# Performance work log

Hardware: AMD Instinct MI355X
Metric: run time of the kernel (lower is better)

Reference implementation:

```python
import jax, jax.numpy as jnp
import numpy as np

B, S, D = 2, 2048, 1024
H, HD = 16, 64          # num_heads, head_dim = D // H
C = 8                   # subspace_dim of the equivariant relative-position basis
EPS = 1e-6              # flax LayerNorm default epsilon


def setup_inputs() -> dict:
    key = jax.random.key(0)
    ks = jax.random.split(key, 12)
    sd = 0.02
    return {
        "x": jax.random.normal(ks[0], (B, S, D), jnp.float32),
        "Q_basis": jax.random.normal(ks[1], (S, S, C), jnp.float32),
        "Wq": jax.random.normal(ks[2], (D, H, HD), jnp.float32) * sd,
        "bq": jnp.zeros((H, HD), jnp.float32),
        "Wk": jax.random.normal(ks[3], (D, H, HD), jnp.float32) * sd,
        "bk": jnp.zeros((H, HD), jnp.float32),
        "Wv": jax.random.normal(ks[4], (D, H, HD), jnp.float32) * sd,
        "bv": jnp.zeros((H, HD), jnp.float32),
        "q_ln_scale": jnp.ones((HD,), jnp.float32),
        "k_ln_scale": jnp.ones((HD,), jnp.float32),
        "relative_attn": jax.random.normal(ks[5], (C, H), jnp.float32) * sd,
        "Wo": jax.random.normal(ks[6], (H, HD, D), jnp.float32) * sd,
        "bo": jnp.zeros((D,), jnp.float32),
    }


def _layernorm(x, scale):
    # LayerNorm over last axis, use_bias=False
    mu = jnp.mean(x, axis=-1, keepdims=True)
    var = jnp.mean(jnp.square(x - mu), axis=-1, keepdims=True)
    return (x - mu) * jax.lax.rsqrt(var + EPS) * scale


def reference(x, Q_basis, Wq, bq, Wk, bk, Wv, bv,
              q_ln_scale, k_ln_scale, relative_attn, Wo, bo):
    # QKV projections: [B,S,D] x [D,H,HD] -> [B,S,H,HD]
    q = jnp.einsum('bsd,dhk->bshk', x, Wq) + bq
    k = jnp.einsum('bsd,dhk->bshk', x, Wk) + bk
    v = jnp.einsum('bsd,dhk->bshk', x, Wv) + bv
    # QK layernorm over head_dim
    q = _layernorm(q, q_ln_scale)
    k = _layernorm(k, k_ln_scale)
    # Learned relative-position bias: [C,H] x [S,S,C] -> [H,S,S]
    bias = jnp.einsum('ch,qkc->hqk', relative_attn, Q_basis)
    # Scaled dot-product attention with bias (matches nn.dot_product_attention)
    scores = jnp.einsum('bqhd,bkhd->bhqk', q, k) / jnp.sqrt(jnp.float32(HD))
    attn = jax.nn.softmax(scores + bias, axis=-1)
    ctx = jnp.einsum('bhqk,bkhd->bqhd', attn, v)
    # Output projection over (heads, head_dim) -> D
    return jnp.einsum('bqhd,hdo->bqo', ctx, Wo) + bo
```

## Files before the change

kernel.cpp:

```cpp
#include <hip/hip_runtime.h>

typedef float f32x4 __attribute__((ext_vector_type(4)));
typedef __bf16 bf16x8 __attribute__((ext_vector_type(8)));
typedef unsigned short u16x8 __attribute__((ext_vector_type(8)));
typedef unsigned short u16x4 __attribute__((ext_vector_type(4)));

#define AS1 __attribute__((address_space(1)))
#define AS3 __attribute__((address_space(3)))

static __device__ __forceinline__ void gll16(const void* g, void* l) {
  __builtin_amdgcn_global_load_lds((const AS1 void*)g, (AS3 void*)l, 16, 0, 0);
}

static __device__ __forceinline__ float bf2f(unsigned short u) {
  unsigned int x = ((unsigned int)u) << 16;
  float f; __builtin_memcpy(&f, &x, 4); return f;
}
static __device__ __forceinline__ unsigned short f2bf(float f) {
  unsigned int x; __builtin_memcpy(&x, &f, 4);
  unsigned int r = (x + 0x7fffu + ((x >> 16) & 1u)) >> 16;
  return (unsigned short)r;
}

#define LOG2E 1.4426950408889634f
#define QSCALE (0.125f * LOG2E)

__global__ __launch_bounds__(256) void k_cvt_x(const float* __restrict__ x,
                                               unsigned short* __restrict__ xb) {
  int i = (blockIdx.x * 256 + threadIdx.x) * 4;
  float4 v = *(const float4*)(x + i);
  u16x4 o; o.x = f2bf(v.x); o.y = f2bf(v.y); o.z = f2bf(v.z); o.w = f2bf(v.w);
  *(u16x4*)(xb + i) = o;
}

__global__ __launch_bounds__(256) void k_transpose(const float* __restrict__ w0,
                                                   const float* __restrict__ w1,
                                                   const float* __restrict__ w2,
                                                   const float* __restrict__ w3,
                                                   unsigned short* __restrict__ dqkv,
                                                   unsigned short* __restrict__ dwo) {
  __shared__ float tile[32][33];
  int z = blockIdx.z;
  const float* src = (z == 0) ? w0 : (z == 1) ? w1 : (z == 2) ? w2 : w3;
  unsigned short* dst = (z < 3) ? (dqkv + (size_t)z * 1024 * 1024) : dwo;
  int tx = threadIdx.x, ty = threadIdx.y;
  int x0 = blockIdx.x * 32, y0 = blockIdx.y * 32;
#pragma unroll
  for (int i = 0; i < 4; ++i)
    tile[ty + 8 * i][tx] = src[(size_t)(y0 + ty + 8 * i) * 1024 + x0 + tx];
  __syncthreads();
#pragma unroll
  for (int i = 0; i < 4; ++i)
    dst[(size_t)(x0 + ty + 8 * i) * 1024 + y0 + tx] = f2bf(tile[tx][ty + 8 * i]);
}

__global__ __launch_bounds__(256) void k_bias(const float* __restrict__ Qb,
                                              const float* __restrict__ R,
                                              unsigned short* __restrict__ bias) {
  __shared__ float Rs[8][16];
  int t = threadIdx.x;
  if (t < 128) Rs[t >> 4][t & 15] = R[t] * LOG2E;
  __syncthreads();
  int q = blockIdx.x;
  int k = t * 8;
  const float* src = Qb + ((size_t)q * 2048 + k) * 8;
  float a[8][8];
#pragma unroll
  for (int kk = 0; kk < 8; ++kk) {
    float4 lo = *(const float4*)(src + kk * 8);
    float4 hi = *(const float4*)(src + kk * 8 + 4);
    a[kk][0] = lo.x; a[kk][1] = lo.y; a[kk][2] = lo.z; a[kk][3] = lo.w;
    a[kk][4] = hi.x; a[kk][5] = hi.y; a[kk][6] = hi.z; a[kk][7] = hi.w;
  }
#pragma unroll
  for (int h = 0; h < 16; ++h) {
    u16x8 o;
#pragma unroll
    for (int kk = 0; kk < 8; ++kk) {
      float s = 0.f;
#pragma unroll
      for (int c = 0; c < 8; ++c) s += a[kk][c] * Rs[c][h];
      o[kk] = f2bf(s);
    }
    *(u16x8*)(bias + ((size_t)h * 2048 + q) * 2048 + k) = o;
  }
}

__global__ __launch_bounds__(256) void k_qkv(const unsigned short* __restrict__ xb,
                                             const unsigned short* __restrict__ wt,
                                             const float* __restrict__ bq,
                                             const float* __restrict__ bk,
                                             const float* __restrict__ bv,
                                             const float* __restrict__ qls,
                                             const float* __restrict__ kls,
                                             unsigned short* __restrict__ qo,
                                             unsigned short* __restrict__ kqo,
                                             unsigned short* __restrict__ vo) {
  __shared__ unsigned short As[4096];
  __shared__ unsigned short Bs[4096];
  const int tid = threadIdx.x;
  const int w = tid >> 6, lane = tid & 63, quad = lane >> 4, lx = lane & 15;
  const int m0 = blockIdx.y * 128, n0 = blockIdx.x * 128;
  const int wrow = w >> 1, wcol = w & 1;

  f32x4 acc[4][4];
#pragma unroll
  for (int i = 0; i < 4; ++i)
#pragma unroll
    for (int j = 0; j < 4; ++j) acc[i][j] = (f32x4){0.f, 0.f, 0.f, 0.f};

  const unsigned short* ga = xb + (size_t)(m0 + 32 * w + (lane >> 2)) * 1024 + (lane & 3) * 8;
  const unsigned short* gb = wt + (size_t)(n0 + 32 * w + (lane >> 2)) * 1024 + (lane & 3) * 8;
  unsigned short* la = As + w * 1024;
  unsigned short* lb = Bs + w * 1024;

  for (int kt = 0; kt < 32; ++kt) {
    const int kofs = kt * 32;
    gll16(ga + kofs, la);
    gll16(ga + kofs + 16 * 1024, la + 512);
    gll16(gb + kofs, lb);
    gll16(gb + kofs + 16 * 1024, lb + 512);
    __syncthreads();
    bf16x8 af[4], bfr[4];
#pragma unroll
    for (int i = 0; i < 4; ++i)
      af[i] = *(const bf16x8*)&As[(64 * wrow + 16 * i + lx) * 32 + quad * 8];
#pragma unroll
    for (int j = 0; j < 4; ++j)
      bfr[j] = *(const bf16x8*)&Bs[(64 * wcol + 16 * j + lx) * 32 + quad * 8];
#pragma unroll
    for (int i = 0; i < 4; ++i)
#pragma unroll
      for (int j = 0; j < 4; ++j)
        acc[i][j] = __builtin_amdgcn_mfma_f32_16x16x32_bf16(af[i], bfr[j], acc[i][j], 0, 0, 0);
    __syncthreads();
  }

  const int colbase = n0 + 64 * wcol;
  const int region = colbase >> 10;
  const int h = (colbase & 1023) >> 6;
  const float* pbp = (region == 0) ? bq : (region == 1) ? bk : bv;
  float pb[4];
#pragma unroll
  for (int j = 0; j < 4; ++j) pb[j] = pbp[h * 64 + j * 16 + lx];

  if (region == 2) {
#pragma unroll
    for (int i = 0; i < 4; ++i) {
#pragma unroll
      for (int rr = 0; rr < 4; ++rr) {
        int m = m0 + 64 * wrow + 16 * i + quad * 4 + rr;
        int b = m >> 11, s = m & 2047;
        unsigned short* dst = vo + ((size_t)b * 16 + h) * 64 * 2048 + s;
#pragma unroll
        for (int j = 0; j < 4; ++j)
          dst[(size_t)(j * 16 + lx) * 2048] = f2bf(acc[i][j][rr] + pb[j]);
      }
    }
  } else {
    const float fac = region ? 1.0f : QSCALE;
    float scl[4];
    const float* lsp = region ? kls : qls;
#pragma unroll
    for (int j = 0; j < 4; ++j) scl[j] = lsp[j * 16 + lx] * fac;
    unsigned short* base = region ? kqo : qo;
#pragma unroll
    for (int i = 0; i < 4; ++i) {
#pragma unroll
      for (int rr = 0; rr < 4; ++rr) {
        int m = m0 + 64 * wrow + 16 * i + quad * 4 + rr;
        int b = m >> 11, s = m & 2047;
        float v0 = acc[i][0][rr] + pb[0];
        float v1 = acc[i][1][rr] + pb[1];
        float v2 = acc[i][2][rr] + pb[2];
        float v3 = acc[i][3][rr] + pb[3];
        float s1 = v0 + v1 + v2 + v3;
        float s2 = v0 * v0 + v1 * v1 + v2 * v2 + v3 * v3;
#pragma unroll
        for (int d = 1; d < 16; d <<= 1) {
          s1 += __shfl_xor(s1, d, 64);
          s2 += __shfl_xor(s2, d, 64);
        }
        float mu = s1 * 0.015625f;
        float var = s2 * 0.015625f - mu * mu;
        float ri = __builtin_amdgcn_rsqf(var + 1e-6f);
        unsigned short* dst = base + (((size_t)b * 16 + h) * 2048 + s) * 64;
        dst[0 * 16 + lx] = f2bf((v0 - mu) * ri * scl[0]);
        dst[1 * 16 + lx] = f2bf((v1 - mu) * ri * scl[1]);
        dst[2 * 16 + lx] = f2bf((v2 - mu) * ri * scl[2]);
        dst[3 * 16 + lx] = f2bf((v3 - mu) * ri * scl[3]);
      }
    }
  }
}

__global__ __launch_bounds__(256) void k_attn(const unsigned short* __restrict__ qp,
                                              const unsigned short* __restrict__ kp,
                                              const unsigned short* __restrict__ vp,
                                              const unsigned short* __restrict__ bp,
                                              unsigned short* __restrict__ ctx) {
  __shared__ unsigned short Qs[4096];
  __shared__ unsigned short Ks[4096];
  __shared__ unsigned short Vs[4096];
  __shared__ unsigned short Ps[4096];
  const int tid = threadIdx.x;
  const int w = tid >> 6, lane = tid & 63, quad = lane >> 4, lx = lane & 15;
  const int qt = blockIdx.x, h = blockIdx.y, b = blockIdx.z;
  const int q0 = qt * 64;
  const size_t bh = (size_t)b * 16 + h;

  const unsigned short* qg = qp + (bh * 2048 + q0) * 64;
  gll16(qg + w * 512 + lane * 8, Qs + w * 512);
  gll16(qg + 2048 + w * 512 + lane * 8, Qs + 2048 + w * 512);
  __syncthreads();
  bf16x8 qf[2];
#pragma unroll
  for (int hh = 0; hh < 2; ++hh)
    qf[hh] = *(const bf16x8*)&Qs[(16 * w + lx) * 64 + hh * 32 + quad * 8];

  const unsigned short* kg = kp + bh * 2048 * 64;
  const unsigned short* vg = vp + bh * 64 * 2048;
  const unsigned short* bg = bp + ((size_t)h * 2048 + q0 + 16 * w + quad * 4) * 2048 + lx;

  float m_run[4] = {-1e30f, -1e30f, -1e30f, -1e30f};
  float l_run[4] = {0.f, 0.f, 0.f, 0.f};
  f32x4 acco[4];
#pragma unroll
  for (int j = 0; j < 4; ++j) acco[j] = (f32x4){0.f, 0.f, 0.f, 0.f};

  for (int kt = 0; kt < 32; ++kt) {
    const int k0 = kt * 64;
    gll16(kg + (size_t)k0 * 64 + w * 512 + lane * 8, Ks + w * 512);
    gll16(kg + (size_t)k0 * 64 + 2048 + w * 512 + lane * 8, Ks + 2048 + w * 512);
    gll16(vg + (size_t)(w * 8 + (lane >> 3)) * 2048 + k0 + (lane & 7) * 8, Vs + w * 512);
    gll16(vg + (size_t)(32 + w * 8 + (lane >> 3)) * 2048 + k0 + (lane & 7) * 8,
          Vs + 2048 + w * 512);
    unsigned short bu[4][4];
#pragma unroll
    for (int rr = 0; rr < 4; ++rr)
#pragma unroll
      for (int j = 0; j < 4; ++j) bu[rr][j] = bg[(size_t)rr * 2048 + k0 + j * 16];
    __syncthreads();

    f32x4 accs[4];
#pragma unroll
    for (int j = 0; j < 4; ++j)
#pragma unroll
      for (int rr = 0; rr < 4; ++rr) accs[j][rr] = bf2f(bu[rr][j]);
#pragma unroll
    for (int j = 0; j < 4; ++j) {
#pragma unroll
      for (int hh = 0; hh < 2; ++hh) {
        bf16x8 kf = *(const bf16x8*)&Ks[(j * 16 + lx) * 64 + hh * 32 + quad * 8];
        accs[j] = __builtin_amdgcn_mfma_f32_16x16x32_bf16(qf[hh], kf, accs[j], 0, 0, 0);
      }
    }
#pragma unroll
    for (int rr = 0; rr < 4; ++rr) {
      float mx = fmaxf(fmaxf(accs[0][rr], accs[1][rr]), fmaxf(accs[2][rr], accs[3][rr]));
#pragma unroll
      for (int d = 1; d < 16; d <<= 1) mx = fmaxf(mx, __shfl_xor(mx, d, 64));
      float mnew = fmaxf(m_run[rr], mx);
      float al = __builtin_amdgcn_exp2f(m_run[rr] - mnew);
      m_run[rr] = mnew;
      float ps = 0.f;
#pragma unroll
      for (int j = 0; j < 4; ++j) {
        float p = __builtin_amdgcn_exp2f(accs[j][rr] - mnew);
        accs[j][rr] = p;
        ps += p;
      }
#pragma unroll
      for (int d = 1; d < 16; d <<= 1) ps += __shfl_xor(ps, d, 64);
      l_run[rr] = l_run[rr] * al + ps;
#pragma unroll
      for (int j = 0; j < 4; ++j) acco[j][rr] *= al;
#pragma unroll
      for (int j = 0; j < 4; ++j)
        Ps[w * 1024 + (quad * 4 + rr) * 64 + j * 16 + lx] = f2bf(accs[j][rr]);
    }
    __asm__ volatile("s_waitcnt lgkmcnt(0)" ::: "memory");
    bf16x8 pf[2];
#pragma unroll
    for (int kh = 0; kh < 2; ++kh)
      pf[kh] = *(const bf16x8*)&Ps[w * 1024 + lx * 64 + kh * 32 + quad * 8];
#pragma unroll
    for (int j = 0; j < 4; ++j) {
#pragma unroll
      for (int kh = 0; kh < 2; ++kh) {
        bf16x8 vf = *(const bf16x8*)&Vs[(j * 16 + lx) * 64 + kh * 32 + quad * 8];
        acco[j] = __builtin_amdgcn_mfma_f32_16x16x32_bf16(pf[kh], vf, acco[j], 0, 0, 0);
      }
    }
    __syncthreads();
  }

#pragma unroll
  for (int rr = 0; rr < 4; ++rr) {
    float rl = __builtin_amdgcn_rcpf(l_run[rr]);
    int s = q0 + 16 * w + quad * 4 + rr;
    unsigned short* dst = ctx + (((size_t)b * 2048 + s) * 16 + h) * 64;
#pragma unroll
    for (int j = 0; j < 4; ++j) dst[j * 16 + lx] = f2bf(acco[j][rr] * rl);
  }
}

__global__ __launch_bounds__(256) void k_out(const unsigned short* __restrict__ cx,
                                             const unsigned short* __restrict__ wt,
                                             const float* __restrict__ bo,
                                             float* __restrict__ out) {
  __shared__ unsigned short As[4096];
  __shared__ unsigned short Bs[4096];
  const int tid = threadIdx.x;
  const int w = tid >> 6, lane = tid & 63, quad = lane >> 4, lx = lane & 15;
  const int m0 = blockIdx.y * 128, n0 = blockIdx.x * 128;
  const int wrow = w >> 1, wcol = w & 1;

  f32x4 acc[4][4];
#pragma unroll
  for (int i = 0; i < 4; ++i)
#pragma unroll
    for (int j = 0; j < 4; ++j) acc[i][j] = (f32x4){0.f, 0.f, 0.f, 0.f};

  const unsigned short* ga = cx + (size_t)(m0 + 32 * w + (lane >> 2)) * 1024 + (lane & 3) * 8;
  const unsigned short* gb = wt + (size_t)(n0 + 32 * w + (lane >> 2)) * 1024 + (lane & 3) * 8;
  unsigned short* la = As + w * 1024;
  unsigned short* lb = Bs + w * 1024;

  for (int kt = 0; kt < 32; ++kt) {
    const int kofs = kt * 32;
    gll16(ga + kofs, la);
    gll16(ga + kofs + 16 * 1024, la + 512);
    gll16(gb + kofs, lb);
    gll16(gb + kofs + 16 * 1024, lb + 512);
    __syncthreads();
    bf16x8 af[4], bfr[4];
#pragma unroll
    for (int i = 0; i < 4; ++i)
      af[i] = *(const bf16x8*)&As[(64 * wrow + 16 * i + lx) * 32 + quad * 8];
#pragma unroll
    for (int j = 0; j < 4; ++j)
      bfr[j] = *(const bf16x8*)&Bs[(64 * wcol + 16 * j + lx) * 32 + quad * 8];
#pragma unroll
    for (int i = 0; i < 4; ++i)
#pragma unroll
      for (int j = 0; j < 4; ++j)
        acc[i][j] = __builtin_amdgcn_mfma_f32_16x16x32_bf16(af[i], bfr[j], acc[i][j], 0, 0, 0);
    __syncthreads();
  }

  const int colbase = n0 + 64 * wcol;
  float bb[4];
#pragma unroll
  for (int j = 0; j < 4; ++j) bb[j] = bo[colbase + j * 16 + lx];
#pragma unroll
  for (int i = 0; i < 4; ++i) {
#pragma unroll
    for (int rr = 0; rr < 4; ++rr) {
      int m = m0 + 64 * wrow + 16 * i + quad * 4 + rr;
      float* dst = out + (size_t)m * 1024 + colbase;
#pragma unroll
      for (int j = 0; j < 4; ++j) dst[j * 16 + lx] = acc[i][j][rr] + bb[j];
    }
  }
}

extern "C" void kernel_launch(void* const* d_in, const int* in_sizes, int n_in,
                              void* d_out, int out_size, void* d_ws, size_t ws_size,
                              hipStream_t stream) {
  (void)in_sizes; (void)n_in; (void)out_size; (void)ws_size;
  const float* x   = (const float*)d_in[0];
  const float* Qb  = (const float*)d_in[1];
  const float* Wq  = (const float*)d_in[2];
  const float* bq  = (const float*)d_in[3];
  const float* Wk  = (const float*)d_in[4];
  const float* bk  = (const float*)d_in[5];
  const float* Wv  = (const float*)d_in[6];
  const float* bv  = (const float*)d_in[7];
  const float* qls = (const float*)d_in[8];
  const float* kls = (const float*)d_in[9];
  const float* Ra  = (const float*)d_in[10];
  const float* Wo  = (const float*)d_in[11];
  const float* bo  = (const float*)d_in[12];
  float* out = (float*)d_out;

  char* ws = (char*)d_ws;
  unsigned short* xb    = (unsigned short*)(ws + 0);
  unsigned short* wqkvt = (unsigned short*)(ws + 8388608);
  unsigned short* wot   = (unsigned short*)(ws + 14680064);
  unsigned short* qb    = (unsigned short*)(ws + 16777216);
  unsigned short* kb    = (unsigned short*)(ws + 25165824);
  unsigned short* vtb   = (unsigned short*)(ws + 33554432);
  unsigned short* ctxb  = (unsigned short*)(ws + 41943040);
  unsigned short* biasb = (unsigned short*)(ws + 50331648);

  k_cvt_x<<<4096, 256, 0, stream>>>(x, xb);
  k_transpose<<<dim3(32, 32, 4), dim3(32, 8), 0, stream>>>(Wq, Wk, Wv, Wo, wqkvt, wot);
  k_bias<<<2048, 256, 0, stream>>>(Qb, Ra, biasb);
  k_qkv<<<dim3(24, 32), 256, 0, stream>>>(xb, wqkvt, bq, bk, bv, qls, kls, qb, kb, vtb);
  k_attn<<<dim3(32, 16, 2), 256, 0, stream>>>(qb, kb, vtb, biasb, ctxb);
  k_out<<<dim3(8, 32), 256, 0, stream>>>(ctxb, wot, bo, out);
}
```

Before: 502.0 us.

## Merge both batches per attention block and drop online-softmax max tracking

Each attention block now handles the same head and query tile for both batch elements, with two waves per batch. This lets the relative-position bias tile be read once per block instead of once per batch, and the grid shrinks to 32x16. The running-max rescaling is removed and the softmax sum is reduced only at the end. That is exact only while the layernormed scores stay small enough not to overflow exp2, which depends on the LN scales. K and V use XOR-swizzled LDS layouts, Q fragments are read straight from global memory, and the MFMA operand order is swapped so bias and P can be loaded and stored as packed vectors.

Result: faster. 461.8 us (-8.0%).

```diff
diff --git a/kernel.cpp b/kernel.cpp
--- a/kernel.cpp
+++ b/kernel.cpp
@@ -199,109 +199,131 @@
                                               const unsigned short* __restrict__ vp,
                                               const unsigned short* __restrict__ bp,
                                               unsigned short* __restrict__ ctx) {
-  __shared__ unsigned short Qs[4096];
-  __shared__ unsigned short Ks[4096];
-  __shared__ unsigned short Vs[4096];
-  __shared__ unsigned short Ps[4096];
+  __shared__ unsigned short Ks[8192];
+  __shared__ unsigned short Vs[8192];
+  __shared__ unsigned short Ps[9216];
   const int tid = threadIdx.x;
   const int w = tid >> 6, lane = tid & 63, quad = lane >> 4, lx = lane & 15;
-  const int qt = blockIdx.x, h = blockIdx.y, b = blockIdx.z;
+  const int bb = w >> 1, ww = w & 1;
+  const int qt = blockIdx.x, h = blockIdx.y;
   const int q0 = qt * 64;
-  const size_t bh = (size_t)b * 16 + h;
-
-  const unsigned short* qg = qp + (bh * 2048 + q0) * 64;
-  gll16(qg + w * 512 + lane * 8, Qs + w * 512);
-  gll16(qg + 2048 + w * 512 + lane * 8, Qs + 2048 + w * 512);
-  __syncthreads();
-  bf16x8 qf[2];
-#pragma unroll
-  for (int hh = 0; hh < 2; ++hh)
-    qf[hh] = *(const bf16x8*)&Qs[(16 * w + lx) * 64 + hh * 32 + quad * 8];
-
-  const unsigned short* kg = kp + bh * 2048 * 64;
-  const unsigned short* vg = vp + bh * 64 * 2048;
-  const unsigned short* bg = bp + ((size_t)h * 2048 + q0 + 16 * w + quad * 4) * 2048 + lx;
-
-  float m_run[4] = {-1e30f, -1e30f, -1e30f, -1e30f};
-  float l_run[4] = {0.f, 0.f, 0.f, 0.f};
-  f32x4 acco[4];
-#pragma unroll
-  for (int j = 0; j < 4; ++j) acco[j] = (f32x4){0.f, 0.f, 0.f, 0.f};
+  const size_t bh = (size_t)bb * 16 + h;
+
+  const unsigned short* qgp = qp + (bh * 2048 + q0 + ww * 32) * 64;
+  bf16x8 qf[2][2];
+#pragma unroll
+  for (int qg = 0; qg < 2; ++qg)
+#pragma unroll
+    for (int hh = 0; hh < 2; ++hh)
+      qf[qg][hh] = *(const bf16x8*)(qgp + (qg * 16 + lx) * 64 + hh * 32 + quad * 8);
+
+  const int r8 = lane >> 3;
+  const int cA = (lane & 7) ^ r8;
+  const unsigned short* kgs = kp + bh * 2048 * 64 + (ww * 32 + r8) * 64 + cA * 8;
+  const unsigned short* vgs = vp + bh * 64 * 2048 + (size_t)(ww * 32 + r8) * 2048 + cA * 8;
+  unsigned short* ldk = Ks + bb * 4096 + ww * 2048;
+  unsigned short* ldv = Vs + bb * 4096 + ww * 2048;
+  const unsigned short* bg = bp + ((size_t)h * 2048 + q0 + ww * 32) * 2048;
+  unsigned short* psw = Ps + w * 2304;
+
+  float l_run[2] = {0.f, 0.f};
+  f32x4 acco[2][4];
+#pragma unroll
+  for (int qg = 0; qg < 2; ++qg)
+#pragma unroll
+    for (int j = 0; j < 4; ++j) acco[qg][j] = (f32x4){0.f, 0.f, 0.f, 0.f};
 
   for (int kt = 0; kt < 32; ++kt) {
     const int k0 = kt * 64;
-    gll16(kg + (size_t)k0 * 64 + w * 512 + lane * 8, Ks + w * 512);
-    gll16(kg + (size_t)k0 * 64 + 2048 + w * 512 + lane * 8, Ks + 2048 + w * 512);
-    gll16(vg + (size_t)(w * 8 + (lane >> 3)) * 2048 + k0 + (lane & 7) * 8, Vs + w * 512);
-    gll16(vg + (size_t)(32 + w * 8 + (lane >> 3)) * 2048 + k0 + (lane & 7) * 8,
-          Vs + 2048 + w * 512);
-    unsigned short bu[4][4];
-#pragma unroll
-    for (int rr = 0; rr < 4; ++rr)
-#pragma unroll
-      for (int j = 0; j < 4; ++j) bu[rr][j] = bg[(size_t)rr * 2048 + k0 + j * 16];
-    __syncthreads();
-
-    f32x4 accs[4];
+#pragma unroll
+    for (int idx = 0; idx < 4; ++idx) {
+      gll16(kgs + (size_t)(k0 + idx * 8) * 64, ldk + idx * 512);
+      gll16(vgs + k0 + idx * 8 * 2048, ldv + idx * 512);
+    }
+    uint2 bu[2][4];
+#pragma unroll
+    for (int qg = 0; qg < 2; ++qg)
+#pragma unroll
+      for (int j = 0; j < 4; ++j)
+        bu[qg][j] = *(const uint2*)(bg + (size_t)(qg * 16 + lx) * 2048 + k0 + j * 16 + quad * 4);
+    __syncthreads();
+
+    bf16x8 kf[4][2];
 #pragma unroll
     for (int j = 0; j < 4; ++j)
 #pragma unroll
-      for (int rr = 0; rr < 4; ++rr) accs[j][rr] = bf2f(bu[rr][j]);
-#pragma unroll
-    for (int j = 0; j < 4; ++j) {
-#pragma unroll
-      for (int hh = 0; hh < 2; ++hh) {
-        bf16x8 kf = *(const bf16x8*)&Ks[(j * 16 + lx) * 64 + hh * 32 + quad * 8];
-        accs[j] = __builtin_amdgcn_mfma_f32_16x16x32_bf16(qf[hh], kf, accs[j], 0, 0, 0);
+      for (int hh = 0; hh < 2; ++hh)
+        kf[j][hh] = *(const bf16x8*)&Ks[bb * 4096 + (j * 16 + lx) * 64 +
+                                        (((hh * 4 + quad) ^ (lx & 7)) * 8)];
+#pragma unroll
+    for (int qg = 0; qg < 2; ++qg) {
+      f32x4 accs[4];
+#pragma unroll
+      for (int j = 0; j < 4; ++j) {
+        accs[j][0] = __uint_as_float(bu[qg][j].x << 16);
+        accs[j][1] = __uint_as_float(bu[qg][j].x & 0xffff0000u);
+        accs[j][2] = __uint_as_float(bu[qg][j].y << 16);
+        accs[j][3] = __uint_as_float(bu[qg][j].y & 0xffff0000u);
       }
-    }
+#pragma unroll
+      for (int hh = 0; hh < 2; ++hh)
+#pragma unroll
+        for (int j = 0; j < 4; ++j)
+          accs[j] = __builtin_amdgcn_mfma_f32_16x16x32_bf16(kf[j][hh], qf[qg][hh], accs[j], 0, 0, 0);
+#pragma unroll
+      for (int j = 0; j < 4; ++j) {
+        float p0 = __builtin_amdgcn_exp2f(accs[j][0]);
+        float p1 = __builtin_amdgcn_exp2f(accs[j][1]);
+        float p2 = __builtin_amdgcn_exp2f(accs[j][2]);
+        float p3 = __builtin_amdgcn_exp2f(accs[j][3]);
+        l_run[qg] += (p0 + p1) + (p2 + p3);
+        unsigned int a0 = __float_as_uint(p0) + 0x8000u;
+        unsigned int a1 = __float_as_uint(p1) + 0x8000u;
+        unsigned int a2 = __float_as_uint(p2) + 0x8000u;
+        unsigned int a3 = __float_as_uint(p3) + 0x8000u;
+        uint2 pk;
+        pk.x = __builtin_amdgcn_perm(a1, a0, 0x07060302u);
+        pk.y = __builtin_amdgcn_perm(a3, a2, 0x07060302u);
+        *(uint2*)&psw[(qg * 16 + lx) * 72 + j * 16 + quad * 4] = pk;
+      }
+    }
+    __asm__ volatile("s_waitcnt lgkmcnt(0)" ::: "memory");
+    bf16x8 vf[4][2];
+#pragma unroll
+    for (int j = 0; j < 4; ++j)
+#pragma unroll
+      for (int kh = 0; kh < 2; ++kh)
+        vf[j][kh] = *(const bf16x8*)&Vs[bb * 4096 + (j * 16 + lx) * 64 +
+                                        (((kh * 4 + quad) ^ (lx & 7)) * 8)];
+#pragma unroll
+    for (int qg = 0; qg < 2; ++qg) {
+      bf16x8 pf[2];
+#pragma unroll
+      for (int kh = 0; kh < 2; ++kh)
+        pf[kh] = *(const bf16x8*)&psw[(qg * 16 + lx) * 72 + kh * 32 + quad * 8];
+#pragma unroll
+      for (int kh = 0; kh < 2; ++kh)
+#pragma unroll
+        for (int j = 0; j < 4; ++j)
+          acco[qg][j] = __builtin_amdgcn_mfma_f32_16x16x32_bf16(pf[kh], vf[j][kh], acco[qg][j], 0, 0, 0);
+    }
+    __syncthreads();
+  }
+
+#pragma unroll
+  for (int qg = 0; qg < 2; ++qg) {
+    float l = l_run[qg];
+    l += __shfl_xor(l, 16, 64);
+    l += __shfl_xor(l, 32, 64);
 #pragma unroll
     for (int rr = 0; rr < 4; ++rr) {
-      float mx = fmaxf(fmaxf(accs[0][rr], accs[1][rr]), fmaxf(accs[2][rr], accs[3][rr]));
-#pragma unroll
-      for (int d = 1; d < 16; d <<= 1) mx = fmaxf(mx, __shfl_xor(mx, d, 64));
-      float mnew = fmaxf(m_run[rr], mx);
-      float al = __builtin_amdgcn_exp2f(m_run[rr] - mnew);
-      m_run[rr] = mnew;
-      float ps = 0.f;
-#pragma unroll
-      for (int j = 0; j < 4; ++j) {
-        float p = __builtin_amdgcn_exp2f(accs[j][rr] - mnew);
-        accs[j][rr] = p;
-        ps += p;
-      }
-#pragma unroll
-      for (int d = 1; d < 16; d <<= 1) ps += __shfl_xor(ps, d, 64);
-      l_run[rr] = l_run[rr] * al + ps;
-#pragma unroll
-      for (int j = 0; j < 4; ++j) acco[j][rr] *= al;
-#pragma unroll
-      for (int j = 0; j < 4; ++j)
-        Ps[w * 1024 + (quad * 4 + rr) * 64 + j * 16 + lx] = f2bf(accs[j][rr]);
-    }
-    __asm__ volatile("s_waitcnt lgkmcnt(0)" ::: "memory");
-    bf16x8 pf[2];
-#pragma unroll
-    for (int kh = 0; kh < 2; ++kh)
-      pf[kh] = *(const bf16x8*)&Ps[w * 1024 + lx * 64 + kh * 32 + quad * 8];
-#pragma unroll
-    for (int j = 0; j < 4; ++j) {
-#pragma unroll
-      for (int kh = 0; kh < 2; ++kh) {
-        bf16x8 vf = *(const bf16x8*)&Vs[(j * 16 + lx) * 64 + kh * 32 + quad * 8];
-        acco[j] = __builtin_amdgcn_mfma_f32_16x16x32_bf16(pf[kh], vf, acco[j], 0, 0, 0);
-      }
-    }
-    __syncthreads();
-  }
-
-#pragma unroll
-  for (int rr = 0; rr < 4; ++rr) {
-    float rl = __builtin_amdgcn_rcpf(l_run[rr]);
-    int s = q0 + 16 * w + quad * 4 + rr;
-    unsigned short* dst = ctx + (((size_t)b * 2048 + s) * 16 + h) * 64;
-#pragma unroll
-    for (int j = 0; j < 4; ++j) dst[j * 16 + lx] = f2bf(acco[j][rr] * rl);
+      float lq = __shfl(l, quad * 4 + rr, 64);
+      float rl = __builtin_amdgcn_rcpf(lq);
+      int q = q0 + ww * 32 + qg * 16 + quad * 4 + rr;
+      unsigned short* dst = ctx + (((size_t)bb * 2048 + q) * 16 + h) * 64;
+#pragma unroll
+      for (int j = 0; j < 4; ++j) dst[j * 16 + lx] = f2bf(acco[qg][j][rr] * rl);
+    }
   }
 }
 
@@ -398,6 +420,6 @@
   k_transpose<<<dim3(32, 32, 4), dim3(32, 8), 0, stream>>>(Wq, Wk, Wv, Wo, wqkvt, wot);
   k_bias<<<2048, 256, 0, stream>>>(Qb, Ra, biasb);
   k_qkv<<<dim3(24, 32), 256, 0, stream>>>(xb, wqkvt, bq, bk, bv, qls, kls, qb, kb, vtb);
-  k_attn<<<dim3(32, 16, 2), 256, 0, stream>>>(qb, kb, vtb, biasb, ctxb);
+  k_attn<<<dim3(32, 16), 256, 0, stream>>>(qb, kb, vtb, biasb, ctxb);
   k_out<<<dim3(8, 32), 256, 0, stream>>>(ctxb, wot, bo, out);
 }
```
